# Optimization experiments

Measured on AMD Instinct MI355X. Metric: run time of the kernel, lower is better.

## Reference

```python
import jax, jax.numpy as jnp
import numpy as np

T, B, H, E, V = 128, 64, 512, 256, 32000
UNK = 2
EPS = 1e-10


def setup_inputs() -> dict:
    key = jax.random.key(0)
    ks = jax.random.split(key, 16)
    s = 0.02
    return {
        "u_enc_out": jax.random.normal(ks[0], (T, B, H), jnp.float32),
        "z_tm1": jax.random.randint(ks[1], (1, B), 0, V),
        "last_hidden": jax.random.normal(ks[2], (1, B, H), jnp.float32),
        "u_input": jax.random.randint(ks[3], (T, B), 0, V),
        "emb": jax.random.normal(ks[4], (V, E), jnp.float32) * s,
        "attn_W": jax.random.normal(ks[5], (H, 2 * H), jnp.float32) * s,
        "attn_b": jnp.zeros((H,), jnp.float32),
        "attn_v": jax.random.normal(ks[6], (H,), jnp.float32) * (1.0 / np.sqrt(H)),
        "gru_Wih": jax.random.normal(ks[7], (3 * H, H + E), jnp.float32) * s,
        "gru_Whh": jax.random.normal(ks[8], (3 * H, H), jnp.float32) * s,
        "gru_bih": jnp.zeros((3 * H,), jnp.float32),
        "gru_bhh": jnp.zeros((3 * H,), jnp.float32),
        "proj_W": jax.random.normal(ks[9], (V, 2 * H), jnp.float32) * s,
        "proj_b": jnp.zeros((V,), jnp.float32),
        "copy1_W": jax.random.normal(ks[10], (H, H), jnp.float32) * s,
        "copy1_b": jnp.zeros((H,), jnp.float32),
    }


def _copy_logscore(raw, u_input):
    # raw: [B,T] copy scores; u_input: [T,B] int ids
    # Faithful to: log(bmm(exp(raw - max), sparse_one_hot_with_1e-10_floor)) + max
    cmax = jnp.max(raw, axis=1, keepdims=True)            # [B,1]
    ex = jnp.exp(raw - cmax)                              # [B,T]
    idx = u_input.T                                       # [B,T]
    idx = jnp.where(idx == UNK, V + jnp.arange(T)[None, :], idx)
    mask = (u_input.T != 0).astype(ex.dtype)
    total = jnp.sum(ex, axis=1)                           # [B] (all t, incl. ignored)
    scat = jax.vmap(lambda e, i: jnp.zeros((V + T,), ex.dtype).at[i].add(e))(ex * mask, idx)
    return jnp.log(EPS * total[:, None] + (1.0 - EPS) * scat) + cmax  # [B,V+T]


def reference(u_enc_out, z_tm1, last_hidden, u_input, emb, attn_W, attn_b, attn_v,
              gru_Wih, gru_Whh, gru_bih, gru_bhh, proj_W, proj_b, copy1_W, copy1_b):
    enc = jnp.transpose(u_enc_out, (1, 0, 2))             # [B,T,H]
    h = last_hidden[0]                                    # [B,H]
    # Attn: energy = tanh(Linear([h;enc])), score = v . energy, softmax over T
    Hrep = jnp.broadcast_to(h[:, None, :], enc.shape)
    energy = jnp.tanh(jnp.einsum('bti,hi->bth', jnp.concatenate([Hrep, enc], -1), attn_W) + attn_b)
    alpha = jax.nn.softmax(jnp.einsum('h,bth->bt', attn_v, energy), axis=1)
    ctx = jnp.einsum('bt,bth->bh', alpha, enc)            # [B,H]
    # GRU step (pytorch gate order r,z,n)
    x = jnp.concatenate([emb[z_tm1[0]], ctx], axis=-1)    # [B,E+H]
    gi = x @ gru_Wih.T + gru_bih
    gh = h @ gru_Whh.T + gru_bhh
    i_r, i_z, i_n = jnp.split(gi, 3, axis=-1)
    h_r, h_z, h_n = jnp.split(gh, 3, axis=-1)
    r = jax.nn.sigmoid(i_r + h_r)
    z = jax.nn.sigmoid(i_z + h_z)
    n = jnp.tanh(i_n + r * h_n)
    h_new = (1.0 - z) * n + z * h                         # [B,H]
    gru_out = h_new[None]                                 # [1,B,H]
    new_hidden = h_new[None]
    # generation score
    gen_score = jnp.concatenate([h_new, ctx], -1) @ proj_W.T + proj_b  # [B,V]
    # copy score
    cs = jnp.tanh(jnp.einsum('bth,ih->bti', enc, copy1_W) + copy1_b)   # [B,T,H]
    raw = jnp.einsum('bth,bh->bt', cs, h_new)             # [B,T]
    u_copy = _copy_logscore(raw, u_input)                 # [B,V+T]
    scores = jax.nn.softmax(jnp.concatenate([gen_score, u_copy], axis=1), axis=1)
    g, c = scores[:, :V], scores[:, V:]                   # [B,V], [B,V+T]
    proba = jnp.concatenate([g + c[:, :V], c[:, V:]], axis=1)  # [B,V+T]
    return gru_out, new_hidden, proba
```

## Files before the change

### kernel.cpp

```cpp
#include <hip/hip_runtime.h>
#include <math.h>

#define T_ 128
#define B_ 64
#define H_ 512
#define E_ 256
#define V_ 32000
#define VT_ (V_ + T_)
#define UNK_ 2
#define EPS_ 1e-10f
#define NP_ (V_ / 64)

typedef __attribute__((ext_vector_type(8))) _Float16 half8;
typedef __attribute__((ext_vector_type(4))) float floatx4;

#define NB_ZERO 32
#define NB_CVTE 2048
#define NB_CVTA 512
#define NB_CVTC 512
#define NB_WH   8192
#define NB_CVTW 2048
#define NB_XE   64
#define NB_XH   128
#define NB_BC   8
#define NB_PRO (NB_ZERO + NB_CVTE + NB_CVTA + NB_CVTC + NB_WH + NB_CVTW + NB_XE + NB_XH + NB_BC)

__global__ __launch_bounds__(256) void prologue_k(
        const float* __restrict__ u_enc, const float* __restrict__ attn_W,
        const float* __restrict__ copy1_W, const float* __restrict__ last_h,
        const float* __restrict__ attn_b, const float* __restrict__ emb,
        const int* __restrict__ z, const float* __restrict__ Wih,
        const float* __restrict__ Whh, const float* __restrict__ bih,
        const float* __restrict__ bhh,
        float* __restrict__ zbase, _Float16* __restrict__ enc_bh,
        _Float16* __restrict__ Wb_attn, _Float16* __restrict__ Wb_copy,
        float* __restrict__ Wh, _Float16* __restrict__ Wcat,
        _Float16* __restrict__ xg, float* __restrict__ bcat) {
    int bid = blockIdx.x, tid = threadIdx.x;
    if (bid < NB_ZERO) { zbase[bid * 256 + tid] = 0.f; return; }
    bid -= NB_ZERO;
    if (bid < NB_CVTE) {
        int idx8 = bid * 256 + tid;
        int i = idx8 * 8;
        float4 a = *(const float4*)(u_enc + i);
        float4 b4 = *(const float4*)(u_enc + i + 4);
        half8 o;
        o[0] = (_Float16)a.x; o[1] = (_Float16)a.y; o[2] = (_Float16)a.z; o[3] = (_Float16)a.w;
        o[4] = (_Float16)b4.x; o[5] = (_Float16)b4.y; o[6] = (_Float16)b4.z; o[7] = (_Float16)b4.w;
        int h8 = idx8 & 63;
        int tb = idx8 >> 6;
        int b = tb & 63, t = tb >> 6;
        *(half8*)(enc_bh + ((size_t)(b * T_ + t) * H_) + h8 * 8) = o;
        return;
    }
    bid -= NB_CVTE;
    if (bid < NB_CVTA) {
        int c = tid * 2;
        float2 v = *(const float2*)(attn_W + (size_t)bid * 1024 + 512 + c);
        Wb_attn[bid * 512 + c]     = (_Float16)v.x;
        Wb_attn[bid * 512 + c + 1] = (_Float16)v.y;
        return;
    }
    bid -= NB_CVTA;
    if (bid < NB_CVTC) {
        int c = tid * 2;
        float2 v = *(const float2*)(copy1_W + (size_t)bid * 512 + c);
        Wb_copy[bid * 512 + c]     = (_Float16)v.x;
        Wb_copy[bid * 512 + c + 1] = (_Float16)v.y;
        return;
    }
    bid -= NB_CVTC;
    if (bid < NB_WH) {
        int wid = bid * 4 + (tid >> 6), lane = tid & 63;
        int b = wid >> 9, m = wid & 511;
        const float4* wr = (const float4*)(attn_W + (size_t)m * 1024);
        const float4* xr = (const float4*)(last_h + b * 512);
        float s = 0.f;
        #pragma unroll
        for (int i = 0; i < 2; ++i) {
            int k = lane + i * 64;
            float4 w = wr[k], x = xr[k];
            s += w.x * x.x + w.y * x.y + w.z * x.z + w.w * x.w;
        }
        #pragma unroll
        for (int off = 32; off > 0; off >>= 1) s += __shfl_down(s, off);
        if (lane == 0) Wh[b * 512 + m] = s + attn_b[m];
        return;
    }
    bid -= NB_WH;
    if (bid < NB_CVTW) {
        int mp = bid;
        int q  = (mp >> 4) & 3;
        int hh = (mp >> 6) * 16 + (mp & 15);
        #pragma unroll
        for (int j = 0; j < 5; ++j) {
            int c = j * 256 + tid;
            float w;
            if (q == 0)      w = (c < 768) ? Wih[(size_t)hh * 768 + c]
                                           : Whh[(size_t)hh * 512 + (c - 768)];
            else if (q == 1) w = (c < 768) ? Wih[(size_t)(512 + hh) * 768 + c]
                                           : Whh[(size_t)(512 + hh) * 512 + (c - 768)];
            else if (q == 2) w = (c < 768) ? Wih[(size_t)(1024 + hh) * 768 + c] : 0.f;
            else             w = (c >= 768) ? Whh[(size_t)(1024 + hh) * 512 + (c - 768)] : 0.f;
            Wcat[(size_t)mp * 1280 + c] = (_Float16)w;
        }
        return;
    }
    bid -= NB_CVTW;
    if (bid < NB_XE) {
        int idx = bid * 256 + tid;
        int bb = idx >> 8, c = idx & 255;
        xg[bb * 1280 + c] = (_Float16)emb[(size_t)z[bb] * E_ + c];
        return;
    }
    bid -= NB_XE;
    if (bid < NB_XH) {
        int idx = bid * 256 + tid;
        int bb = idx >> 9, c = idx & 511;
        xg[bb * 1280 + 768 + c] = (_Float16)last_h[bb * H_ + c];
        return;
    }
    bid -= NB_XH;
    {
        int mp = bid * 256 + tid;
        int q  = (mp >> 4) & 3;
        int hh = (mp >> 6) * 16 + (mp & 15);
        float v2;
        if (q == 0)      v2 = bih[hh] + bhh[hh];
        else if (q == 1) v2 = bih[512 + hh] + bhh[512 + hh];
        else if (q == 2) v2 = bih[1024 + hh];
        else             v2 = bhh[1024 + hh];
        bcat[mp] = v2;
    }
}

__global__ __launch_bounds__(256) void enc_dual_k(
        const _Float16* __restrict__ enc_bh,
        const _Float16* __restrict__ Wa,
        const _Float16* __restrict__ Wc,
        const float* __restrict__ Wh,
        const float* __restrict__ attn_v,
        const float* __restrict__ copy1_b,
        float* __restrict__ score,
        _Float16* __restrict__ cs) {
    __shared__ _Float16 As[64 * 512];
    int bid = blockIdx.x;
    int xcd = bid & 7, loc = bid >> 3;
    int xt = xcd * 16 + (loc & 15);
    int yt = loc >> 4;
    int r0 = xt * 64;
    int b  = r0 >> 7;
    int tid = threadIdx.x;
    int lane = tid & 63, wave = tid >> 6;
    const half8* src = (const half8*)(enc_bh + (size_t)r0 * H_);
    #pragma unroll
    for (int i = 0; i < 16; ++i) {
        int G = i * 256 + tid;
        half8 v = src[G];
        int r = G >> 6, s = G & 63;
        *(half8*)&As[(size_t)(((r << 6) | (s ^ (r & 7))) << 3)] = v;
    }
    __syncthreads();
    int n0 = yt * 64 + wave * 16;
    int coln = lane & 15;
    int g = lane >> 4;
    const _Float16* wra = Wa + (size_t)(n0 + coln) * H_ + g * 8;
    const _Float16* wrc = Wc + (size_t)(n0 + coln) * H_ + g * 8;
    floatx4 acca[4] = {}, accc[4] = {};
    #pragma unroll 4
    for (int k0 = 0; k0 < H_; k0 += 32) {
        half8 fba = *(const half8*)(wra + k0);
        half8 fbc = *(const half8*)(wrc + k0);
        #pragma unroll
        for (int mi = 0; mi < 4; ++mi) {
            int r = mi * 16 + coln;
            half8 fa = *(const half8*)&As[((size_t)r << 9) +
                          ((((k0 >> 3) + g) ^ (coln & 7)) << 3)];
            acca[mi] = __builtin_amdgcn_mfma_f32_16x16x32_f16(fa, fba, acca[mi], 0, 0, 0);
            accc[mi] = __builtin_amdgcn_mfma_f32_16x16x32_f16(fa, fbc, accc[mi], 0, 0, 0);
        }
    }
    int col = n0 + coln;
    float addt = Wh[b * H_ + col];
    float av   = attn_v[col];
    float cb   = copy1_b[col];
    int rbase = g * 4;
    #pragma unroll
    for (int mi = 0; mi < 4; ++mi)
        #pragma unroll
        for (int r = 0; r < 4; ++r) {
            int row = r0 + mi * 16 + rbase + r;
            float x = acca[mi][r] + addt;
            float t2 = __expf(2.f * x);
            float v = av * ((t2 - 1.f) / (t2 + 1.f));
            v += __shfl_xor(v, 1);
            v += __shfl_xor(v, 2);
            v += __shfl_xor(v, 4);
            v += __shfl_xor(v, 8);
            if (coln == 0) atomicAdd(&score[row], v);
            float y = accc[mi][r] + cb;
            float t3 = __expf(2.f * y);
            cs[(size_t)row * H_ + col] = (_Float16)((t3 - 1.f) / (t3 + 1.f));
        }
}

__global__ __launch_bounds__(256) void softctx_k(
        const float* __restrict__ score, const _Float16* __restrict__ enc_bh,
        _Float16* __restrict__ xcat, _Float16* __restrict__ xg) {
    __shared__ float al[T_];
    __shared__ float red[T_];
    int b = blockIdx.x, tid = threadIdx.x;
    float v = (tid < T_) ? score[b * T_ + tid] : -1e30f;
    if (tid < T_) red[tid] = v;
    __syncthreads();
    for (int s = 64; s > 0; s >>= 1) { if (tid < s) red[tid] = fmaxf(red[tid], red[tid + s]); __syncthreads(); }
    float m = red[0]; __syncthreads();
    float e = (tid < T_) ? __expf(v - m) : 0.f;
    if (tid < T_) red[tid] = e;
    __syncthreads();
    for (int s = 64; s > 0; s >>= 1) { if (tid < s) red[tid] += red[tid + s]; __syncthreads(); }
    if (tid < T_) al[tid] = e / red[0];
    __syncthreads();
    int h = blockIdx.y * 256 + tid;
    float s2 = 0.f;
    #pragma unroll 4
    for (int t = 0; t < T_; ++t) s2 += al[t] * (float)enc_bh[((size_t)b * T_ + t) * H_ + h];
    xcat[b * 1024 + 512 + h] = (_Float16)s2;
    xg[b * 1280 + 256 + h]   = (_Float16)s2;
}

__global__ __launch_bounds__(256) void grucat_k(
        const _Float16* __restrict__ xg,
        const _Float16* __restrict__ Wcat,
        const float* __restrict__ bcat,
        const float* __restrict__ hprev,
        float* __restrict__ out,
        _Float16* __restrict__ xcat) {
    __shared__ float Lt[4][64][16];
    int lane = threadIdx.x & 63;
    int wave = threadIdx.x >> 6;
    int n0 = blockIdx.x * 64 + wave * 16;
    int coln = lane & 15;
    int kq  = (lane >> 4) * 8;
    const _Float16* wrow = Wcat + (size_t)(n0 + coln) * 1280 + kq;
    const _Float16* abase = xg + kq;
    floatx4 acc[4] = {};
    #pragma unroll 8
    for (int k0 = 0; k0 < 1280; k0 += 32) {
        half8 fb = *(const half8*)(wrow + k0);
        #pragma unroll
        for (int mi = 0; mi < 4; ++mi) {
            half8 fa = *(const half8*)(abase + (size_t)(mi * 16 + coln) * 1280 + k0);
            acc[mi] = __builtin_amdgcn_mfma_f32_16x16x32_f16(fa, fb, acc[mi], 0, 0, 0);
        }
    }
    int rbase = (lane >> 4) * 4;
    float bias = bcat[n0 + coln];
    #pragma unroll
    for (int mi = 0; mi < 4; ++mi)
        #pragma unroll
        for (int r = 0; r < 4; ++r)
            Lt[wave][mi * 16 + rbase + r][coln] = acc[mi][r] + bias;
    __syncthreads();
    int HB = blockIdx.x * 16;
    #pragma unroll
    for (int p = threadIdx.x; p < 1024; p += 256) {
        int b = p >> 4, i = p & 15;
        float rr = 1.f / (1.f + __expf(-Lt[0][b][i]));
        float zz = 1.f / (1.f + __expf(-Lt[1][b][i]));
        float nn = tanhf(Lt[2][b][i] + rr * Lt[3][b][i]);
        float h  = hprev[b * H_ + HB + i];
        float hv = (1.f - zz) * nn + zz * h;
        out[b * H_ + HB + i] = hv;
        out[B_ * H_ + b * H_ + HB + i] = hv;
        xcat[b * 1024 + HB + i] = (_Float16)hv;
    }
}

__global__ __launch_bounds__(256) void proj_stats_k(
        const _Float16* __restrict__ xcat,
        const float* __restrict__ Wp,
        const float* __restrict__ bp,
        float* __restrict__ gen,
        float* __restrict__ mpart, float* __restrict__ lpart) {
    __shared__ float m_lds[4][64];
    __shared__ float l_lds[4][64];
    int lane = threadIdx.x & 63;
    int wave = threadIdx.x >> 6;
    int n0 = (blockIdx.x * 4 + wave) * 16;
    int coln = lane & 15;
    int kq  = (lane >> 4) * 8;
    const float* wrow = Wp + (size_t)(n0 + coln) * 1024 + kq;
    const _Float16* abase = xcat + kq;
    floatx4 acc[4] = {};
    #pragma unroll 8
    for (int k0 = 0; k0 < 1024; k0 += 32) {
        const float4* wb = (const float4*)(wrow + k0);
        float4 w0 = wb[0], w1 = wb[1];
        half8 fb;
        fb[0] = (_Float16)w0.x; fb[1] = (_Float16)w0.y; fb[2] = (_Float16)w0.z; fb[3] = (_Float16)w0.w;
        fb[4] = (_Float16)w1.x; fb[5] = (_Float16)w1.y; fb[6] = (_Float16)w1.z; fb[7] = (_Float16)w1.w;
        #pragma unroll
        for (int mi = 0; mi < 4; ++mi) {
            half8 fa = *(const half8*)(abase + (size_t)(mi * 16 + coln) * 1024 + k0);
            acc[mi] = __builtin_amdgcn_mfma_f32_16x16x32_f16(fa, fb, acc[mi], 0, 0, 0);
        }
    }
    int rbase = (lane >> 4) * 4;
    float bias = bp[n0 + coln];
    #pragma unroll
    for (int mi = 0; mi < 4; ++mi)
        #pragma unroll
        for (int r = 0; r < 4; ++r) {
            int brow = mi * 16 + rbase + r;
            float x = acc[mi][r] + bias;
            gen[(size_t)brow * V_ + n0 + coln] = x;
            float mm = x;
            mm = fmaxf(mm, __shfl_xor(mm, 1));
            mm = fmaxf(mm, __shfl_xor(mm, 2));
            mm = fmaxf(mm, __shfl_xor(mm, 4));
            mm = fmaxf(mm, __shfl_xor(mm, 8));
            float e = __expf(x - mm);
            e += __shfl_xor(e, 1);
            e += __shfl_xor(e, 2);
            e += __shfl_xor(e, 4);
            e += __shfl_xor(e, 8);
            if (coln == 0) { m_lds[wave][brow] = mm; l_lds[wave][brow] = e; }
        }
    __syncthreads();
    if (threadIdx.x < 64) {
        int bb = threadIdx.x;
        float M = m_lds[0][bb], L = l_lds[0][bb];
        #pragma unroll
        for (int w = 1; w < 4; ++w) {
            float m2 = m_lds[w][bb], l2 = l_lds[w][bb];
            float nm = fmaxf(M, m2);
            L = L * __expf(M - nm) + l2 * __expf(m2 - nm);
            M = nm;
        }
        mpart[bb * NP_ + blockIdx.x] = M;
        lpart[bb * NP_ + blockIdx.x] = L;
    }
}

__global__ __launch_bounds__(256) void raw_epi_k(
        const _Float16* __restrict__ cs, const float* __restrict__ hnew,
        const int* __restrict__ u_input,
        const float* __restrict__ mpart, const float* __restrict__ lpart,
        float* __restrict__ scat, float* __restrict__ params) {
    __shared__ float rawS[T_];
    __shared__ float red[T_];
    __shared__ float ms[256], ls[256];
    int b = blockIdx.x, tid = threadIdx.x;
    int lane = tid & 63, wave = tid >> 6;
    const float4* hp = (const float4*)(hnew + b * H_ + lane * 8);
    float4 ha = hp[0], hb = hp[1];
    #pragma unroll 4
    for (int i = 0; i < 32; ++i) {
        int t = wave * 32 + i;
        half8 c8 = *(const half8*)(cs + (size_t)(b * T_ + t) * H_ + lane * 8);
        float s = (float)c8[0] * ha.x + (float)c8[1] * ha.y + (float)c8[2] * ha.z + (float)c8[3] * ha.w
                + (float)c8[4] * hb.x + (float)c8[5] * hb.y + (float)c8[6] * hb.z + (float)c8[7] * hb.w;
        #pragma unroll
        for (int off = 32; off > 0; off >>= 1) s += __shfl_down(s, off);
        if (lane == 0) rawS[t] = s;
    }
    __syncthreads();
    int t = tid;
    float v = (t < T_) ? rawS[t] : -1e30f;
    if (t < T_) red[t] = v;
    __syncthreads();
    for (int s = 64; s > 0; s >>= 1) { if (t < s) red[t] = fmaxf(red[t], red[t + s]); __syncthreads(); }
    float cm = red[0]; __syncthreads();
    float e = (t < T_) ? __expf(v - cm) : 0.f;
    if (t < T_) red[t] = e;
    __syncthreads();
    for (int s = 64; s > 0; s >>= 1) { if (t < s) red[t] += red[t + s]; __syncthreads(); }
    float tot = red[0]; __syncthreads();
    int id = (t < T_) ? u_input[t * B_ + b] : 0;
    size_t j = (size_t)b * VT_ + ((id == UNK_) ? (V_ + t) : id);
    if (id != 0) scat[j] = 0.f;
    __syncthreads();
    if (id != 0) atomicAdd(&scat[j], e);
    if (t < T_) red[t] = (id != 0) ? e : 0.f;
    __syncthreads();
    for (int s = 64; s > 0; s >>= 1) { if (t < s) red[t] += red[t + s]; __syncthreads(); }
    float ssum = red[0]; __syncthreads();
    float sv = (id != 0) ? scat[j] : 0.f;
    if (t < T_) red[t] = sv;
    __syncthreads();
    for (int s = 64; s > 0; s >>= 1) { if (t < s) red[t] = fmaxf(red[t], red[t + s]); __syncthreads(); }
    float smax = red[0]; __syncthreads();
    float M = -1e30f, L = 0.f;
    for (int s = t; s < NP_; s += 256) {
        float m2 = mpart[b * NP_ + s], l2 = lpart[b * NP_ + s];
        float nm = fmaxf(M, m2);
        L = L * __expf(M - nm) + l2 * __expf(m2 - nm);
        M = nm;
    }
    ms[t] = M; ls[t] = L;
    __syncthreads();
    for (int s = 128; s > 0; s >>= 1) {
        if (t < s) {
            float m2 = ms[t + s], l2 = ls[t + s];
            float nm = fmaxf(ms[t], m2);
            ls[t] = ls[t] * __expf(ms[t] - nm) + l2 * __expf(m2 - nm);
            ms[t] = nm;
        }
        __syncthreads();
    }
    if (t == 0) {
        float Mg = ms[0], Zg = ls[0];
        float umax = cm + logf(EPS_ * tot + (1.f - EPS_) * smax);
        float M2 = fmaxf(Mg, umax);
        float coef = __expf(cm - M2);
        float Z = Zg * __expf(Mg - M2) + coef * (EPS_ * tot * (float)VT_ + (1.f - EPS_) * ssum);
        float invZ = 1.f / Z;
        params[b * 4 + 0] = M2;
        params[b * 4 + 1] = invZ;
        params[b * 4 + 2] = coef * EPS_ * tot * invZ;
        params[b * 4 + 3] = coef * (1.f - EPS_) * invZ;
    }
}

__global__ __launch_bounds__(256) void write_k(const float* __restrict__ gen,
                                               const float* __restrict__ params,
                                               float* __restrict__ proba) {
    int b = blockIdx.y;
    int i4 = blockIdx.x * 256 + threadIdx.x;
    if (i4 >= VT_ / 4) return;
    float M = params[b * 4], invZ = params[b * 4 + 1], addc = params[b * 4 + 2];
    int j = i4 * 4;
    float4 p;
    if (j < V_) {
        float4 g = *(const float4*)(gen + (size_t)b * V_ + j);
        p.x = addc + __expf(g.x - M) * invZ;
        p.y = addc + __expf(g.y - M) * invZ;
        p.z = addc + __expf(g.z - M) * invZ;
        p.w = addc + __expf(g.w - M) * invZ;
    } else {
        p.x = p.y = p.z = p.w = addc;
    }
    *(float4*)(proba + (size_t)b * VT_ + j) = p;
}

__global__ void fix_k(const float* __restrict__ gen, const float* __restrict__ scat,
                      const int* __restrict__ u_input, const float* __restrict__ params,
                      float* __restrict__ proba) {
    int b = blockIdx.x, t = threadIdx.x;
    int id = u_input[t * B_ + b];
    if (id == 0) return;
    int j = (id == UNK_) ? (V_ + t) : id;
    float M = params[b * 4], invZ = params[b * 4 + 1];
    float addc = params[b * 4 + 2], scoef = params[b * 4 + 3];
    float p = addc + scoef * scat[(size_t)b * VT_ + j];
    if (j < V_) p += __expf(gen[(size_t)b * V_ + j] - M) * invZ;
    proba[(size_t)b * VT_ + j] = p;
}

extern "C" void kernel_launch(void* const* d_in, const int* in_sizes, int n_in,
                              void* d_out, int out_size, void* d_ws, size_t ws_size,
                              hipStream_t stream) {
    const float* u_enc   = (const float*)d_in[0];
    const int*   z_tm1   = (const int*)d_in[1];
    const float* last_h  = (const float*)d_in[2];
    const int*   u_input = (const int*)d_in[3];
    const float* emb     = (const float*)d_in[4];
    const float* attn_W  = (const float*)d_in[5];
    const float* attn_b  = (const float*)d_in[6];
    const float* attn_v  = (const float*)d_in[7];
    const float* gru_Wih = (const float*)d_in[8];
    const float* gru_Whh = (const float*)d_in[9];
    const float* gru_bih = (const float*)d_in[10];
    const float* gru_bhh = (const float*)d_in[11];
    const float* proj_W  = (const float*)d_in[12];
    const float* proj_b  = (const float*)d_in[13];
    const float* copy1_W = (const float*)d_in[14];
    const float* copy1_b = (const float*)d_in[15];
    float* out = (float*)d_out;

    float* ws    = (float*)d_ws;
    float* score = ws;
    float* gen   = score + B_ * T_;
    float* scat  = gen + (size_t)B_ * V_;
    float* Wh    = scat + (size_t)B_ * VT_;
    float* mpart = Wh + B_ * H_;
    float* lpart = mpart + B_ * NP_;
    float* params= lpart + B_ * NP_;
    float* bcat  = params + B_ * 4;
    _Float16* xcat  = (_Float16*)(bcat + 2048);
    _Float16* xg    = xcat + B_ * 1024;
    _Float16* enc_bh = xg + B_ * 1280;
    _Float16* Wb_attn = enc_bh + (size_t)T_ * B_ * H_;
    _Float16* Wb_copy = Wb_attn + H_ * H_;
    _Float16* Wcat  = Wb_copy + H_ * H_;
    _Float16* cs    = Wcat + 2048 * 1280;

    prologue_k<<<NB_PRO, 256, 0, stream>>>(u_enc, attn_W, copy1_W, last_h, attn_b,
                                           emb, z_tm1, gru_Wih, gru_Whh, gru_bih, gru_bhh,
                                           score, enc_bh, Wb_attn, Wb_copy, Wh, Wcat, xg, bcat);

    enc_dual_k<<<1024, 256, 0, stream>>>(enc_bh, Wb_attn, Wb_copy, Wh, attn_v, copy1_b,
                                         score, cs);

    softctx_k<<<dim3(B_, 2), 256, 0, stream>>>(score, enc_bh, xcat, xg);

    grucat_k<<<2048 / 64, 256, 0, stream>>>(xg, Wcat, bcat, last_h, out, xcat);

    proj_stats_k<<<NP_, 256, 0, stream>>>(xcat, proj_W, proj_b, gen, mpart, lpart);

    raw_epi_k<<<B_, 256, 0, stream>>>(cs, out, u_input, mpart, lpart, scat, params);

    float* proba = out + 2 * B_ * H_;
    write_k<<<dim3((VT_ / 4 + 255) / 256, B_), 256, 0, stream>>>(gen, params, proba);
    fix_k<<<B_, T_, 0, stream>>>(gen, scat, u_input, params, proba);
}
```

Baseline: 372.7 us.

## Use MFMA for attention Wh, split-K GRU gemm, vectorize context sum

Replaces the 8192-block wave-per-output dot product for W·h in the prologue with 8 blocks computing the same product via fp16 MFMA, converting fp32 inputs on the fly. The GRU gemm now uses 512 threads with split-K over two halves, summed through padded LDS. The context reduction processes two halves per thread with one block per batch row. This lowers the fp32 Wh precision to fp16 and concentrates Wh work onto few blocks, which may leave that segment long-running.

```diff
diff --git a/kernel.cpp b/kernel.cpp
--- a/kernel.cpp
+++ b/kernel.cpp
@@ -12,18 +12,19 @@
 #define NP_ (V_ / 64)
 
 typedef __attribute__((ext_vector_type(8))) _Float16 half8;
+typedef __attribute__((ext_vector_type(2))) _Float16 half2v;
 typedef __attribute__((ext_vector_type(4))) float floatx4;
 
 #define NB_ZERO 32
 #define NB_CVTE 2048
 #define NB_CVTA 512
 #define NB_CVTC 512
-#define NB_WH   8192
+#define NB_WHM  8
 #define NB_CVTW 2048
 #define NB_XE   64
 #define NB_XH   128
 #define NB_BC   8
-#define NB_PRO (NB_ZERO + NB_CVTE + NB_CVTA + NB_CVTC + NB_WH + NB_CVTW + NB_XE + NB_XH + NB_BC)
+#define NB_PRO (NB_ZERO + NB_CVTE + NB_CVTA + NB_CVTC + NB_WHM + NB_CVTW + NB_XE + NB_XH + NB_BC)
 
 __global__ __launch_bounds__(256) void prologue_k(
         const float* __restrict__ u_enc, const float* __restrict__ attn_W,
@@ -70,24 +71,41 @@
         return;
     }
     bid -= NB_CVTC;
-    if (bid < NB_WH) {
-        int wid = bid * 4 + (tid >> 6), lane = tid & 63;
-        int b = wid >> 9, m = wid & 511;
-        const float4* wr = (const float4*)(attn_W + (size_t)m * 1024);
-        const float4* xr = (const float4*)(last_h + b * 512);
-        float s = 0.f;
-        #pragma unroll
-        for (int i = 0; i < 2; ++i) {
-            int k = lane + i * 64;
-            float4 w = wr[k], x = xr[k];
-            s += w.x * x.x + w.y * x.y + w.z * x.z + w.w * x.w;
-        }
-        #pragma unroll
-        for (int off = 32; off > 0; off >>= 1) s += __shfl_down(s, off);
-        if (lane == 0) Wh[b * 512 + m] = s + attn_b[m];
-        return;
-    }
-    bid -= NB_WH;
+    if (bid < NB_WHM) {
+        int lane = tid & 63, wave = tid >> 6;
+        int n0 = bid * 64 + wave * 16;
+        int coln = lane & 15;
+        int kq = (lane >> 4) * 8;
+        const float* wrow = attn_W + (size_t)(n0 + coln) * 1024 + kq;
+        const float* arow0 = last_h + kq;
+        floatx4 acc[4] = {};
+        #pragma unroll 4
+        for (int k0 = 0; k0 < 512; k0 += 32) {
+            const float4* wb = (const float4*)(wrow + k0);
+            float4 w0 = wb[0], w1 = wb[1];
+            half8 fb;
+            fb[0] = (_Float16)w0.x; fb[1] = (_Float16)w0.y; fb[2] = (_Float16)w0.z; fb[3] = (_Float16)w0.w;
+            fb[4] = (_Float16)w1.x; fb[5] = (_Float16)w1.y; fb[6] = (_Float16)w1.z; fb[7] = (_Float16)w1.w;
+            #pragma unroll
+            for (int mi = 0; mi < 4; ++mi) {
+                const float4* ab = (const float4*)(arow0 + (size_t)(mi * 16 + coln) * 512 + k0);
+                float4 a0 = ab[0], a1 = ab[1];
+                half8 fa;
+                fa[0] = (_Float16)a0.x; fa[1] = (_Float16)a0.y; fa[2] = (_Float16)a0.z; fa[3] = (_Float16)a0.w;
+                fa[4] = (_Float16)a1.x; fa[5] = (_Float16)a1.y; fa[6] = (_Float16)a1.z; fa[7] = (_Float16)a1.w;
+                acc[mi] = __builtin_amdgcn_mfma_f32_16x16x32_f16(fa, fb, acc[mi], 0, 0, 0);
+            }
+        }
+        int rbase = (lane >> 4) * 4;
+        float bias = attn_b[n0 + coln];
+        #pragma unroll
+        for (int mi = 0; mi < 4; ++mi)
+            #pragma unroll
+            for (int r = 0; r < 4; ++r)
+                Wh[(size_t)(mi * 16 + rbase + r) * 512 + n0 + coln] = acc[mi][r] + bias;
+        return;
+    }
+    bid -= NB_WHM;
     if (bid < NB_CVTW) {
         int mp = bid;
         int q  = (mp >> 4) & 3;
@@ -221,32 +239,41 @@
     for (int s = 64; s > 0; s >>= 1) { if (tid < s) red[tid] += red[tid + s]; __syncthreads(); }
     if (tid < T_) al[tid] = e / red[0];
     __syncthreads();
-    int h = blockIdx.y * 256 + tid;
-    float s2 = 0.f;
-    #pragma unroll 4
-    for (int t = 0; t < T_; ++t) s2 += al[t] * (float)enc_bh[((size_t)b * T_ + t) * H_ + h];
-    xcat[b * 1024 + 512 + h] = (_Float16)s2;
-    xg[b * 1280 + 256 + h]   = (_Float16)s2;
-}
-
-__global__ __launch_bounds__(256) void grucat_k(
+    const half2v* ebase = (const half2v*)(enc_bh + (size_t)b * T_ * H_) + tid;
+    float s0 = 0.f, s1 = 0.f;
+    #pragma unroll 8
+    for (int t = 0; t < T_; ++t) {
+        half2v u = ebase[(size_t)t * 256];
+        float a = al[t];
+        s0 += a * (float)u[0];
+        s1 += a * (float)u[1];
+    }
+    int h0 = tid * 2;
+    half2v o; o[0] = (_Float16)s0; o[1] = (_Float16)s1;
+    *(half2v*)(xcat + b * 1024 + 512 + h0) = o;
+    *(half2v*)(xg + b * 1280 + 256 + h0)   = o;
+}
+
+__global__ __launch_bounds__(512) void grucat_k(
         const _Float16* __restrict__ xg,
         const _Float16* __restrict__ Wcat,
         const float* __restrict__ bcat,
         const float* __restrict__ hprev,
         float* __restrict__ out,
         _Float16* __restrict__ xcat) {
-    __shared__ float Lt[4][64][16];
-    int lane = threadIdx.x & 63;
-    int wave = threadIdx.x >> 6;
-    int n0 = blockIdx.x * 64 + wave * 16;
+    __shared__ float Lt[8][64][17];
+    int tid = threadIdx.x;
+    int lane = tid & 63, wave = tid >> 6;
+    int q = wave & 3, khalf = wave >> 2;
+    int n0 = blockIdx.x * 64 + q * 16;
     int coln = lane & 15;
     int kq  = (lane >> 4) * 8;
-    const _Float16* wrow = Wcat + (size_t)(n0 + coln) * 1280 + kq;
-    const _Float16* abase = xg + kq;
+    int kbase = khalf * 640;
+    const _Float16* wrow  = Wcat + (size_t)(n0 + coln) * 1280 + kbase + kq;
+    const _Float16* abase = xg + kbase + kq;
     floatx4 acc[4] = {};
-    #pragma unroll 8
-    for (int k0 = 0; k0 < 1280; k0 += 32) {
+    #pragma unroll 5
+    for (int k0 = 0; k0 < 640; k0 += 32) {
         half8 fb = *(const half8*)(wrow + k0);
         #pragma unroll
         for (int mi = 0; mi < 4; ++mi) {
@@ -255,20 +282,23 @@
         }
     }
     int rbase = (lane >> 4) * 4;
-    float bias = bcat[n0 + coln];
     #pragma unroll
     for (int mi = 0; mi < 4; ++mi)
         #pragma unroll
         for (int r = 0; r < 4; ++r)
-            Lt[wave][mi * 16 + rbase + r][coln] = acc[mi][r] + bias;
+            Lt[wave][mi * 16 + rbase + r][coln] = acc[mi][r];
     __syncthreads();
     int HB = blockIdx.x * 16;
     #pragma unroll
-    for (int p = threadIdx.x; p < 1024; p += 256) {
+    for (int p = tid; p < 1024; p += 512) {
         int b = p >> 4, i = p & 15;
-        float rr = 1.f / (1.f + __expf(-Lt[0][b][i]));
-        float zz = 1.f / (1.f + __expf(-Lt[1][b][i]));
-        float nn = tanhf(Lt[2][b][i] + rr * Lt[3][b][i]);
+        float G0 = Lt[0][b][i] + Lt[4][b][i] + bcat[blockIdx.x * 64 + i];
+        float G1 = Lt[1][b][i] + Lt[5][b][i] + bcat[blockIdx.x * 64 + 16 + i];
+        float G2 = Lt[2][b][i] + Lt[6][b][i] + bcat[blockIdx.x * 64 + 32 + i];
+        float G3 = Lt[3][b][i] + Lt[7][b][i] + bcat[blockIdx.x * 64 + 48 + i];
+        float rr = 1.f / (1.f + __expf(-G0));
+        float zz = 1.f / (1.f + __expf(-G1));
+        float nn = tanhf(G2 + rr * G3);
         float h  = hprev[b * H_ + HB + i];
         float hv = (1.f - zz) * nn + zz * h;
         out[b * H_ + HB + i] = hv;
@@ -503,9 +533,9 @@
     enc_dual_k<<<1024, 256, 0, stream>>>(enc_bh, Wb_attn, Wb_copy, Wh, attn_v, copy1_b,
                                          score, cs);
 
-    softctx_k<<<dim3(B_, 2), 256, 0, stream>>>(score, enc_bh, xcat, xg);
-
-    grucat_k<<<2048 / 64, 256, 0, stream>>>(xg, Wcat, bcat, last_h, out, xcat);
+    softctx_k<<<B_, 256, 0, stream>>>(score, enc_bh, xcat, xg);
+
+    grucat_k<<<32, 512, 0, stream>>>(xg, Wcat, bcat, last_h, out, xcat);
 
     proj_stats_k<<<NP_, 256, 0, stream>>>(xcat, proj_W, proj_b, gen, mpart, lpart);
 
```

Result: slower. 381.6 us (+2.4%).
